# Kernel tuning notes

Measured on AMD Instinct MI355X. Metric: run time of the kernel, lower is better.

Reference implementation:

```python
import jax, jax.numpy as jnp
import numpy as np

N = 50000      # nodes
E = 800000     # edges
F = 128        # node_features
DSS = 64       # degree_set_size
H = 128        # latent dim (hardcoded in GraphES)


def gcn_conv(x, W, b, src, dst, n):
    # PyG GCNConv: linear -> symmetric-normalized aggregation with self loops -> bias
    h = x @ W                                            # [N, C_out]
    deg = jnp.zeros((n,), x.dtype).at[dst].add(1.0) + 1.0  # in-degree incl. self loop
    dinv = jax.lax.rsqrt(deg)
    norm = dinv[src] * dinv[dst]                         # [E]
    agg = jnp.zeros_like(h).at[dst].add(h[src] * norm[:, None])
    agg = agg + h * (dinv * dinv)[:, None]               # self-loop term (norm_ii = 1/deg_i)
    return agg + b


def mlp(x, w1, b1, w2, b2):
    return jax.nn.relu(x @ w1 + b1) @ w2 + b2


def _swap(ei, i1, i2, coin):
    e1 = jnp.take(ei, i1, axis=1)
    e2 = jnp.take(ei, i2, axis=1)
    a, b = e1[0], e1[1]
    c, d = e2[0], e2[1]
    ne1 = jnp.where(coin, jnp.stack([a, d]), jnp.stack([a, c]))
    ne2 = jnp.where(coin, jnp.stack([c, b]), jnp.stack([b, d]))
    return ei.at[:, i1].set(ne1).at[:, i2].set(ne2)


def setup_inputs() -> dict:
    key = jax.random.key(0)
    ks = jax.random.split(key, 24)
    s = 0.05

    def rn(k, shape):
        return jax.random.normal(k, shape, jnp.float32) * s

    return {
        "x": jax.random.normal(ks[0], (N, F), jnp.float32),
        "edge_index": jax.random.randint(ks[1], (2, E), 0, N, dtype=jnp.int32),
        "degree_set": jax.random.randint(ks[2], (N,), 0, DSS, dtype=jnp.int32),
        "timesteps": 5,
        # encoder: GCN(F+DSS -> 2H), GCN(2H -> H)
        "enc_w1": rn(ks[3], (F + DSS, 2 * H)), "enc_b1": jnp.zeros((2 * H,), jnp.float32),
        "enc_w2": rn(ks[4], (2 * H, H)),       "enc_b2": jnp.zeros((H,), jnp.float32),
        # decoder: GCN(H+DSS -> 2F), GCN(2F -> F)
        "dec_w1": rn(ks[5], (H + DSS, 2 * F)), "dec_b1": jnp.zeros((2 * F,), jnp.float32),
        "dec_w2": rn(ks[6], (2 * F, F)),       "dec_b2": jnp.zeros((F,), jnp.float32),
        # edge_predictor_1: Linear(128,64)->ReLU->Linear(64,1)
        "ep1_w1": rn(ks[7], (H, 64)),  "ep1_b1": jnp.zeros((64,), jnp.float32),
        "ep1_w2": rn(ks[8], (64, 1)),  "ep1_b2": jnp.zeros((1,), jnp.float32),
        # edge_predictor_2: input is z concat flattened pair features -> 128+256=384
        "ep2_w1": rn(ks[9], (H + 2 * H, 64)), "ep2_b1": jnp.zeros((64,), jnp.float32),
        "ep2_w2": rn(ks[10], (64, 1)),        "ep2_b2": jnp.zeros((1,), jnp.float32),
    }


def reference(x, edge_index, degree_set, timesteps,
              enc_w1, enc_b1, enc_w2, enc_b2,
              dec_w1, dec_b1, dec_w2, dec_b2,
              ep1_w1, ep1_b1, ep1_w2, ep1_b2,
              ep2_w1, ep2_b1, ep2_w2, ep2_b2):
    src, dst = edge_index[0], edge_index[1]
    dh = jax.nn.one_hot(degree_set, DSS, dtype=x.dtype)  # [N, DSS]

    # ---- encoder ----
    h = jax.nn.relu(gcn_conv(jnp.concatenate([x, dh], 1), enc_w1, enc_b1, src, dst, N))
    z = gcn_conv(h, enc_w2, enc_b2, src, dst, N)          # [N, H]

    # ---- forward diffusion: timesteps random edge swaps (deterministic PRNG) ----
    ei = edge_index
    for t in range(timesteps):
        k1, k2 = jax.random.split(jax.random.fold_in(jax.random.key(1), t))
        idx = jax.random.choice(k1, E, (2,), replace=False)
        ei = _swap(ei, idx[0], idx[1], jax.random.bernoulli(k2))

    # ---- reverse process: argmax-driven edge swaps ----
    # edge_predictor_1 scores depend only on z -> identical every step; compute once
    i1 = jnp.argmax(mlp(z, ep1_w1, ep1_b1, ep1_w2, ep1_b2).squeeze(-1))
    for t in range(timesteps):
        e1 = jnp.take(ei, i1, axis=1)                     # [2]
        e1f = z[e1].reshape(-1)                           # [2H]
        cond = jnp.concatenate([z, jnp.broadcast_to(e1f, (N, 2 * H))], 1)
        i2 = jnp.argmax(mlp(cond, ep2_w1, ep2_b1, ep2_w2, ep2_b2).squeeze(-1))
        coin = jax.random.bernoulli(jax.random.fold_in(jax.random.key(2), t))
        ei = _swap(ei, i1, i2, coin)

    # ---- decoder on final edge structure ----
    src2, dst2 = ei[0], ei[1]
    hd = jax.nn.relu(gcn_conv(jnp.concatenate([z, dh], 1), dec_w1, dec_b1, src2, dst2, N))
    out = gcn_conv(hd, dec_w2, dec_b2, src2, dst2, N)     # [N, F]
    return out, ei
```

## Files before the change

kernel.cpp:

```cpp
#include <hip/hip_runtime.h>
#include <cstdint>
#include <cstddef>
#include <vector>
#include <algorithm>

#define NN 50000
#define EE 800000
#define FF 128
#define HH 128
#define TSTEPS 5

typedef __attribute__((ext_vector_type(8))) short bf16x8;
typedef __attribute__((ext_vector_type(4))) float f32x4;

__device__ __forceinline__ float bf2f(unsigned short u)
{
    return __uint_as_float((unsigned)u << 16);
}
__device__ __forceinline__ unsigned short f2bf(float x)
{
    unsigned u = __float_as_uint(x);
    u = (u + 0x7FFFu + ((u >> 16) & 1u));
    return (unsigned short)(u >> 16);
}
__device__ __forceinline__ void splitbf(float v, unsigned short& hi, unsigned short& lo)
{
    hi = f2bf(v);
    lo = f2bf(v - bf2f(hi));
}

__device__ __forceinline__ void gload16(const void* g, void* l)
{
    __builtin_amdgcn_global_load_lds(
        (const __attribute__((address_space(1))) void*)g,
        (__attribute__((address_space(3))) void*)l, 16, 0, 0);
}

template <int K, int C, bool HAS_BIAS, bool OUTBF16, bool RELU>
__global__ __launch_bounds__(256) void gemm_rw(
    const float* __restrict__ A, const float* __restrict__ W,
    void* __restrict__ Pout, int n, const float* __restrict__ bias)
{
    constexpr int RPW = 8, ROWS = 32, CG = C / 64;
    __shared__ float As[ROWS][K];
    const int row0 = blockIdx.x * ROWS;
    const int tid = threadIdx.x;
    for (int idx4 = tid; idx4 < ROWS * K / 4; idx4 += 256) {
        int idx = idx4 * 4;
        int r = idx / K, k = idx - r * K;
        int gr = row0 + r;
        float4 v = make_float4(0.f, 0.f, 0.f, 0.f);
        if (gr < n) v = *(const float4*)(A + (size_t)gr * K + k);
        As[r][k + 0] = v.x; As[r][k + 1] = v.y;
        As[r][k + 2] = v.z; As[r][k + 3] = v.w;
    }
    __syncthreads();
    const int w = tid >> 6, l = tid & 63;
    float acc[RPW][CG];
#pragma unroll
    for (int r = 0; r < RPW; r++)
#pragma unroll
        for (int c = 0; c < CG; c++) acc[r][c] = 0.f;

    for (int k = 0; k < K; k++) {
        float wv[CG];
#pragma unroll
        for (int c = 0; c < CG; c++) wv[c] = W[k * C + l + 64 * c];
#pragma unroll
        for (int r = 0; r < RPW; r++) {
            float a = As[w * RPW + r][k];
#pragma unroll
            for (int c = 0; c < CG; c++) acc[r][c] = fmaf(a, wv[c], acc[r][c]);
        }
    }
#pragma unroll
    for (int r = 0; r < RPW; r++) {
        int gr = row0 + w * RPW + r;
        if (gr >= n) continue;
#pragma unroll
        for (int c = 0; c < CG; c++) {
            int col = l + 64 * c;
            float v = acc[r][c];
            if (HAS_BIAS) v += bias[col];
            if (RELU)     v = fmaxf(v, 0.f);
            if (OUTBF16) ((unsigned short*)Pout)[(size_t)gr * C + col] = f2bf(v);
            else         ((float*)Pout)[(size_t)gr * C + col] = v;
        }
    }
}

template <int K, int C, bool HAS_BIAS, bool RELU>
__global__ __launch_bounds__(256) void gemm_mfma(
    const unsigned short* __restrict__ A, const unsigned short* __restrict__ Wp,
    unsigned short* __restrict__ Pout, const float* __restrict__ bias, int n)
{
    constexpr int KC = K / 32;
    constexpr int NT = C / 16;
    __shared__ unsigned short As[64][K];
    const int row0 = blockIdx.x * 64;
    const int tid = threadIdx.x;
    for (int idx = tid; idx < 64 * (K / 8); idx += 256) {
        int r = idx / (K / 8), k8 = idx - r * (K / 8);
        int gr = row0 + r;
        bf16x8 v = { 0, 0, 0, 0, 0, 0, 0, 0 };
        if (gr < n) v = *(const bf16x8*)(A + (size_t)gr * K + k8 * 8);
        *(bf16x8*)(&As[r][k8 * 8]) = v;
    }
    __syncthreads();
    const int w = tid >> 6, lane = tid & 63;
    const int m = lane & 15, quad = lane >> 4;
    const int rowBase = w * 16;

    f32x4 acc[NT];
#pragma unroll
    for (int t = 0; t < NT; t++) acc[t] = { 0.f, 0.f, 0.f, 0.f };

    for (int kc = 0; kc < KC; kc++) {
        bf16x8 a = *(const bf16x8*)(&As[rowBase + m][kc * 32 + quad * 8]);
#pragma unroll
        for (int t = 0; t < NT; t++) {
            int ncol = t * 16 + m;
            bf16x8 b = *(const bf16x8*)(Wp + ((size_t)kc * C + ncol) * 32 + quad * 8);
            acc[t] = __builtin_amdgcn_mfma_f32_16x16x32_bf16(a, b, acc[t], 0, 0, 0);
        }
    }
#pragma unroll
    for (int t = 0; t < NT; t++) {
        int col = t * 16 + m;
#pragma unroll
        for (int r = 0; r < 4; r++) {
            int gr = row0 + rowBase + quad * 4 + r;
            if (gr >= n) continue;
            float v = acc[t][r];
            if (HAS_BIAS) v += bias[col];
            if (RELU)     v = fmaxf(v, 0.f);
            Pout[(size_t)gr * C + col] = f2bf(v);
        }
    }
}

template <int K, int C, int BC, int WR, int WC, bool HAS_BIAS, bool RELU, bool OUT_SPLIT>
__global__ __launch_bounds__(256) void gemm_split_tiled(
    const unsigned short* __restrict__ Ahi, const unsigned short* __restrict__ Alo,
    const unsigned short* __restrict__ Whi, const unsigned short* __restrict__ Wlo,
    void* __restrict__ PoutHi, unsigned short* __restrict__ PoutLo,
    const float* __restrict__ bias, int n)
{
    constexpr int KC = K / 32;
    constexpr int RT = 128 / (WR * 16);
    constexpr int TT = BC / (WC * 16);
    constexpr int LDS_USHORTS = 8192 + BC * 64;
    __shared__ __align__(16) unsigned short smem[LDS_USHORTS];
    unsigned short* AhL = smem;
    unsigned short* AlL = smem + 4096;
    unsigned short* WhL = smem + 8192;
    unsigned short* WlL = smem + 8192 + BC * 32;

    const int row0 = blockIdx.x * 128;
    const int col0 = blockIdx.y * BC;
    const int tid = threadIdx.x;
    const int w = tid >> 6, l = tid & 63;
    const int m = l & 15, quad = l >> 4;
    const int wr = w / WC, wc = w % WC;
    const int rowBase = wr * (RT * 16);
    const int colBase = wc * (TT * 16);

    f32x4 acc[RT][TT];
#pragma unroll
    for (int rt = 0; rt < RT; rt++)
#pragma unroll
        for (int tt = 0; tt < TT; tt++) acc[rt][tt] = { 0.f, 0.f, 0.f, 0.f };

    for (int kc = 0; kc < KC; kc++) {
        for (int s = w; s < 8; s += 4) {
            int rg = row0 + s * 16 + (l >> 2);
            if (rg > n - 1) rg = n - 1;
            size_t go = (size_t)rg * K + kc * 32 + (l & 3) * 8;
            gload16(Ahi + go, AhL + s * 512);
            gload16(Alo + go, AlL + s * 512);
        }
        for (int s = w; s < BC / 16; s += 4) {
            size_t wo = ((size_t)kc * C + col0) * 32 + s * 512 + l * 8;
            gload16(Whi + wo, WhL + s * 512);
            gload16(Wlo + wo, WlL + s * 512);
        }
        __syncthreads();

        bf16x8 ah[RT], al[RT];
#pragma unroll
        for (int rt = 0; rt < RT; rt++) {
            int ro = (rowBase + rt * 16 + m) * 32 + quad * 8;
            ah[rt] = *(const bf16x8*)(AhL + ro);
            al[rt] = *(const bf16x8*)(AlL + ro);
        }
#pragma unroll
        for (int tt = 0; tt < TT; tt++) {
            int co = (colBase + tt * 16 + m) * 32 + quad * 8;
            bf16x8 wh = *(const bf16x8*)(WhL + co);
            bf16x8 wl = *(const bf16x8*)(WlL + co);
#pragma unroll
            for (int rt = 0; rt < RT; rt++) {
                acc[rt][tt] = __builtin_amdgcn_mfma_f32_16x16x32_bf16(al[rt], wh, acc[rt][tt], 0, 0, 0);
                acc[rt][tt] = __builtin_amdgcn_mfma_f32_16x16x32_bf16(ah[rt], wl, acc[rt][tt], 0, 0, 0);
                acc[rt][tt] = __builtin_amdgcn_mfma_f32_16x16x32_bf16(ah[rt], wh, acc[rt][tt], 0, 0, 0);
            }
        }
        __syncthreads();
    }

    if (OUT_SPLIT) {
        unsigned short* Ot = smem;
#pragma unroll
        for (int tt = 0; tt < TT; tt++) {
            int col_in = colBase + tt * 16 + m;
            float bv = HAS_BIAS ? bias[col0 + col_in] : 0.f;
#pragma unroll
            for (int rt = 0; rt < RT; rt++)
#pragma unroll
                for (int r = 0; r < 4; r++) {
                    int row_in = rowBase + rt * 16 + quad * 4 + r;
                    float v = acc[rt][tt][r] + bv;
                    if (RELU) v = fmaxf(v, 0.f);
                    Ot[row_in * BC + col_in] = f2bf(v);
                }
        }
        __syncthreads();
        for (int idx = tid; idx < 128 * (BC / 8); idx += 256) {
            int rr = idx / (BC / 8), c8 = idx - rr * (BC / 8);
            int gr = row0 + rr;
            if (gr < n)
                *(bf16x8*)((unsigned short*)PoutHi + (size_t)gr * C + col0 + c8 * 8) =
                    *(const bf16x8*)(Ot + rr * BC + c8 * 8);
        }
        __syncthreads();
#pragma unroll
        for (int tt = 0; tt < TT; tt++) {
            int col_in = colBase + tt * 16 + m;
            float bv = HAS_BIAS ? bias[col0 + col_in] : 0.f;
#pragma unroll
            for (int rt = 0; rt < RT; rt++)
#pragma unroll
                for (int r = 0; r < 4; r++) {
                    int row_in = rowBase + rt * 16 + quad * 4 + r;
                    float v = acc[rt][tt][r] + bv;
                    if (RELU) v = fmaxf(v, 0.f);
                    unsigned short h = f2bf(v);
                    Ot[row_in * BC + col_in] = f2bf(v - bf2f(h));
                }
        }
        __syncthreads();
        for (int idx = tid; idx < 128 * (BC / 8); idx += 256) {
            int rr = idx / (BC / 8), c8 = idx - rr * (BC / 8);
            int gr = row0 + rr;
            if (gr < n)
                *(bf16x8*)(PoutLo + (size_t)gr * C + col0 + c8 * 8) =
                    *(const bf16x8*)(Ot + rr * BC + c8 * 8);
        }
    } else {
#pragma unroll
        for (int tt = 0; tt < TT; tt++) {
            int col = col0 + colBase + tt * 16 + m;
            float bv = HAS_BIAS ? bias[col] : 0.f;
#pragma unroll
            for (int rt = 0; rt < RT; rt++)
#pragma unroll
                for (int r = 0; r < 4; r++) {
                    int gr = row0 + rowBase + rt * 16 + quad * 4 + r;
                    if (gr >= n) continue;
                    float v = acc[rt][tt][r] + bv;
                    if (RELU) v = fmaxf(v, 0.f);
                    ((float*)PoutHi)[(size_t)gr * C + col] = v;
                }
        }
    }
}

template <int K, int C>
__global__ void pack_w(const float* __restrict__ W, unsigned short* __restrict__ Wp)
{
    int idx = blockIdx.x * 256 + threadIdx.x;
    if (idx >= K * C) return;
    int k = idx / C, nn = idx - k * C;
    Wp[((size_t)(k >> 5) * C + nn) * 32 + (k & 31)] = f2bf(W[idx]);
}

template <int K, int C>
__global__ void pack_w_split(const float* __restrict__ W,
                             unsigned short* __restrict__ Wphi,
                             unsigned short* __restrict__ Wplo)
{
    int idx = blockIdx.x * 256 + threadIdx.x;
    if (idx >= K * C) return;
    int k = idx / C, nn = idx - k * C;
    unsigned short hi, lo;
    splitbf(W[idx], hi, lo);
    size_t o = ((size_t)(k >> 5) * C + nn) * 32 + (k & 31);
    Wphi[o] = hi;
    Wplo[o] = lo;
}

__global__ void count_deg(const int* __restrict__ dst, int* __restrict__ cnt, int e)
{
    int i = blockIdx.x * blockDim.x + threadIdx.x;
    if (i < e) {
        unsigned d = (unsigned)dst[i];
        if (d < (unsigned)NN) atomicAdd(&cnt[d], 1);
    }
}

__global__ void make_dinv(const int* __restrict__ cnt, float* __restrict__ dinv, int n)
{
    int i = blockIdx.x * blockDim.x + threadIdx.x;
    if (i < n) dinv[i] = 1.0f / sqrtf((float)cnt[i] + 1.0f);
}

__global__ void scan_block(const int* __restrict__ cnt, int* __restrict__ excl,
                           int* __restrict__ bsum, int n)
{
    __shared__ int s[256];
    int i = blockIdx.x * 256 + threadIdx.x;
    int v = (i < n) ? cnt[i] : 0;
    s[threadIdx.x] = v;
    __syncthreads();
    for (int off = 1; off < 256; off <<= 1) {
        int t = (threadIdx.x >= off) ? s[threadIdx.x - off] : 0;
        __syncthreads();
        s[threadIdx.x] += t;
        __syncthreads();
    }
    if (i < n) excl[i] = s[threadIdx.x] - v;
    if (threadIdx.x == 255) bsum[blockIdx.x] = s[255];
}
__global__ void scan_bsum(int* __restrict__ bsum, int nb)
{
    if (threadIdx.x || blockIdx.x) return;
    int acc = 0;
    for (int b = 0; b < nb; b++) { int t = bsum[b]; bsum[b] = acc; acc += t; }
}
__global__ void scan_add(int* __restrict__ rowptr, const int* __restrict__ bsum, int n, int e)
{
    int i = blockIdx.x * 256 + threadIdx.x;
    if (i < n) rowptr[i] += bsum[blockIdx.x];
    if (i == 0) rowptr[n] = e;
}

__global__ void csr_fill_pairs(const int* __restrict__ src, const int* __restrict__ dst,
                               const float* __restrict__ dinv, const int* __restrict__ rowptr,
                               int* __restrict__ fill, int* __restrict__ csr_src,
                               float* __restrict__ csr_nrm, int e)
{
    int i = blockIdx.x * blockDim.x + threadIdx.x;
    if (i >= e) return;
    int d = dst[i], s = src[i];
    if ((unsigned)d >= (unsigned)NN || (unsigned)s >= (unsigned)NN) return;
    int slot = rowptr[d] + atomicAdd(&fill[d], 1);
    csr_src[slot] = s;
    csr_nrm[slot] = dinv[s] * dinv[d];
}

template <bool BF16SRC, int OUTMODE>
__global__ __launch_bounds__(256) void agg_feat(
    const void* __restrict__ Xv, const int* __restrict__ ds,
    const int* __restrict__ rowptr, const int* __restrict__ csr_src,
    const float* __restrict__ csr_nrm, const float* __restrict__ dinv,
    void* __restrict__ Fout, unsigned short* __restrict__ FoutLo)
{
    const int w = threadIdx.x >> 6, l = threadIdx.x & 63;
    const int i = blockIdx.x * 4 + w;
    if (i >= NN) return;
    const int half = l >> 5, lh = l & 31;

    auto loadRow4 = [&](int s, float* v) {
        if (BF16SRC) {
            ushort4 u = ((const ushort4*)((const unsigned short*)Xv + (size_t)s * 128))[lh];
            v[0] = bf2f(u.x); v[1] = bf2f(u.y); v[2] = bf2f(u.z); v[3] = bf2f(u.w);
        } else {
            float4 t = ((const float4*)((const float*)Xv + (size_t)s * 128))[lh];
            v[0] = t.x; v[1] = t.y; v[2] = t.z; v[3] = t.w;
        }
    };

    float di = dinv[i], d2 = di * di;
    float acc[4];
    {
        float sv[4];
        loadRow4(i, sv);
        float wgt = half ? 0.f : d2;
#pragma unroll
        for (int v = 0; v < 4; v++) acc[v] = sv[v] * wgt;
    }
    float hist = (ds[i] == l) ? d2 : 0.f;

    const int beg = rowptr[i], end = rowptr[i + 1];
    int idx = beg;
    for (; idx + 8 <= end; idx += 8) {
        int s[8]; float nw[8]; int b[8];
#pragma unroll
        for (int j = 0; j < 8; j++) { s[j] = csr_src[idx + j]; nw[j] = csr_nrm[idx + j]; }
#pragma unroll
        for (int j = 0; j < 8; j++) b[j] = ds[s[j]];
        float vv[4][4];
#pragma unroll
        for (int p = 0; p < 4; p++) loadRow4(s[2 * p + half], vv[p]);
#pragma unroll
        for (int p = 0; p < 4; p++) {
            float wp = nw[2 * p + half];
#pragma unroll
            for (int v = 0; v < 4; v++) acc[v] = fmaf(vv[p][v], wp, acc[v]);
        }
#pragma unroll
        for (int j = 0; j < 8; j++) hist += (b[j] == l) ? nw[j] : 0.f;
    }
    for (; idx + 2 <= end; idx += 2) {
        int s0 = csr_src[idx], s1 = csr_src[idx + 1];
        float n0 = csr_nrm[idx], n1 = csr_nrm[idx + 1];
        int b0 = ds[s0], b1 = ds[s1];
        float v0[4];
        loadRow4(half ? s1 : s0, v0);
        float wp = half ? n1 : n0;
#pragma unroll
        for (int v = 0; v < 4; v++) acc[v] = fmaf(v0[v], wp, acc[v]);
        hist += (b0 == l) ? n0 : 0.f;
        hist += (b1 == l) ? n1 : 0.f;
    }
    if (idx < end) {
        int s0 = csr_src[idx];
        float n0 = csr_nrm[idx];
        int b0 = ds[s0];
        float v0[4];
        loadRow4(s0, v0);
        float wp = half ? 0.f : n0;
#pragma unroll
        for (int v = 0; v < 4; v++) acc[v] = fmaf(v0[v], wp, acc[v]);
        hist += (b0 == l) ? n0 : 0.f;
    }
#pragma unroll
    for (int v = 0; v < 4; v++) acc[v] += __shfl_xor(acc[v], 32, 64);

    if (OUTMODE == 2) {
        if (half == 0) {
            unsigned short h[4], lo[4];
#pragma unroll
            for (int v = 0; v < 4; v++) splitbf(acc[v], h[v], lo[v]);
            ((ushort4*)((unsigned short*)Fout + (size_t)i * 192))[lh] =
                make_ushort4(h[0], h[1], h[2], h[3]);
            ((ushort4*)(FoutLo + (size_t)i * 192))[lh] =
                make_ushort4(lo[0], lo[1], lo[2], lo[3]);
        }
        unsigned short hh, ll;
        splitbf(hist, hh, ll);
        ((unsigned short*)Fout)[(size_t)i * 192 + 128 + l] = hh;
        FoutLo[(size_t)i * 192 + 128 + l] = ll;
    } else if (OUTMODE == 1) {
        if (half == 0) {
            ((ushort4*)((unsigned short*)Fout + (size_t)i * 192))[lh] =
                make_ushort4(f2bf(acc[0]), f2bf(acc[1]), f2bf(acc[2]), f2bf(acc[3]));
        }
        ((unsigned short*)Fout)[(size_t)i * 192 + 128 + l] = f2bf(hist);
    } else {
        if (half == 0) {
            ((float4*)((float*)Fout + (size_t)i * 192))[lh] =
                make_float4(acc[0], acc[1], acc[2], acc[3]);
        }
        ((float*)Fout)[(size_t)i * 192 + 128 + l] = hist;
    }
}

template <bool RELU, bool BF16P>
__global__ __launch_bounds__(256) void agg_wave(
    const void* __restrict__ Pv, const int* __restrict__ rowptr,
    const int* __restrict__ csr_src, const float* __restrict__ csr_nrm,
    const float* __restrict__ dinv, const float* __restrict__ bias,
    float* __restrict__ B, unsigned short* __restrict__ Bbf)
{
    const int w = threadIdx.x >> 6, l = threadIdx.x & 63;
    const int i = blockIdx.x * 4 + w;
    if (i >= NN) return;
    const int half = l >> 5, lh = l & 31;

    auto loadRow4 = [&](int s, float* v) {
        if (BF16P) {
            ushort4 u = ((const ushort4*)((const unsigned short*)Pv + (size_t)s * 128))[lh];
            v[0] = bf2f(u.x); v[1] = bf2f(u.y); v[2] = bf2f(u.z); v[3] = bf2f(u.w);
        } else {
            float4 t = ((const float4*)((const float*)Pv + (size_t)s * 128))[lh];
            v[0] = t.x; v[1] = t.y; v[2] = t.z; v[3] = t.w;
        }
    };

    float di = dinv[i], d2 = di * di;
    float acc[4];
    {
        float sv[4];
        loadRow4(i, sv);
        float wgt = half ? 0.f : d2;
#pragma unroll
        for (int v = 0; v < 4; v++) acc[v] = sv[v] * wgt;
    }

    const int beg = rowptr[i], end = rowptr[i + 1];
    int idx = beg;
    for (; idx + 8 <= end; idx += 8) {
        int s[8]; float nw[8];
#pragma unroll
        for (int j = 0; j < 8; j++) { s[j] = csr_src[idx + j]; nw[j] = csr_nrm[idx + j]; }
        float vv[4][4];
#pragma unroll
        for (int p = 0; p < 4; p++) loadRow4(s[2 * p + half], vv[p]);
#pragma unroll
        for (int p = 0; p < 4; p++) {
            float wp = nw[2 * p + half];
#pragma unroll
            for (int v = 0; v < 4; v++) acc[v] = fmaf(vv[p][v], wp, acc[v]);
        }
    }
    for (; idx + 2 <= end; idx += 2) {
        int s0 = csr_src[idx], s1 = csr_src[idx + 1];
        float n0 = csr_nrm[idx], n1 = csr_nrm[idx + 1];
        float v0[4];
        loadRow4(half ? s1 : s0, v0);
        float wp = half ? n1 : n0;
#pragma unroll
        for (int v = 0; v < 4; v++) acc[v] = fmaf(v0[v], wp, acc[v]);
    }
    if (idx < end) {
        int s0 = csr_src[idx];
        float n0 = csr_nrm[idx];
        float v0[4];
        loadRow4(s0, v0);
        float wp = half ? 0.f : n0;
#pragma unroll
        for (int v = 0; v < 4; v++) acc[v] = fmaf(v0[v], wp, acc[v]);
    }
#pragma unroll
    for (int v = 0; v < 4; v++) acc[v] += __shfl_xor(acc[v], 32, 64);

    if (half == 0) {
        float r[4];
#pragma unroll
        for (int v = 0; v < 4; v++) {
            r[v] = acc[v] + bias[lh * 4 + v];
            if (RELU) r[v] = fmaxf(r[v], 0.f);
        }
        ((float4*)(B + (size_t)i * 128))[lh] = make_float4(r[0], r[1], r[2], r[3]);
        if (Bbf)
            ((ushort4*)(Bbf + (size_t)i * 128))[lh] =
                make_ushort4(f2bf(r[0]), f2bf(r[1]), f2bf(r[2]), f2bf(r[3]));
    }
}

__device__ __forceinline__ unsigned long long packScore(float s, int i)
{
    unsigned u = __float_as_uint(s);
    u = (u & 0x80000000u) ? ~u : (u | 0x80000000u);
    return ((unsigned long long)u << 32) | (unsigned)(~(unsigned)i);
}
__device__ __forceinline__ int unpackIdx(unsigned long long v)
{
    return (int)(~(unsigned)(v & 0xFFFFFFFFull));
}
__device__ __forceinline__ unsigned long long maxu64(unsigned long long a,
                                                     unsigned long long b)
{
    return a > b ? a : b;
}

__global__ __launch_bounds__(256) void score1_blocks(
    const float* __restrict__ z, const float* __restrict__ w1,
    const float* __restrict__ b1, const float* __restrict__ w2,
    unsigned long long* __restrict__ blockBest, int n)
{
    __shared__ float Zs[16][HH];
    __shared__ float W1s[HH * 64];
    __shared__ float W2s[64], B1s[64];
    __shared__ unsigned long long red[4];
    const int row0 = blockIdx.x * 16;
    const int tid = threadIdx.x;
    for (int idx = tid; idx < 16 * HH; idx += 256) {
        int r = idx >> 7, k = idx & 127;
        int gr = row0 + r;
        Zs[r][k] = (gr < n) ? z[(size_t)gr * HH + k] : 0.f;
    }
    for (int idx = tid; idx < HH * 64; idx += 256) W1s[idx] = w1[idx];
    if (tid < 64) { W2s[tid] = w2[tid]; B1s[tid] = b1[tid]; }
    __syncthreads();

    const int w = tid >> 6, l = tid & 63;
    float acc[4];
#pragma unroll
    for (int r = 0; r < 4; r++) acc[r] = B1s[l];
#pragma unroll 16
    for (int k = 0; k < HH; k++) {
        float wv = W1s[k * 64 + l];
#pragma unroll
        for (int r = 0; r < 4; r++)
            acc[r] = fmaf(Zs[w * 4 + r][k], wv, acc[r]);
    }
    unsigned long long best = 0;
#pragma unroll
    for (int r = 0; r < 4; r++) {
        float p = fmaxf(acc[r], 0.f) * W2s[l];
#pragma unroll
        for (int off = 32; off > 0; off >>= 1) p += __shfl_xor(p, off, 64);
        int row = row0 + w * 4 + r;
        if (row < n) best = maxu64(best, packScore(p, row));
    }
    if (l == 0) red[w] = best;
    __syncthreads();
    if (tid == 0)
        blockBest[blockIdx.x] = maxu64(maxu64(red[0], red[1]), maxu64(red[2], red[3]));
}

__global__ __launch_bounds__(256) void reduce_best(
    const unsigned long long* __restrict__ arr, int m,
    unsigned long long* __restrict__ out)
{
    __shared__ unsigned long long red[4];
    const int tid = threadIdx.x;
    unsigned long long b = 0;
    for (int i = tid; i < m; i += 256) b = maxu64(b, arr[i]);
#pragma unroll
    for (int off = 32; off > 0; off >>= 1)
        b = maxu64(b, (unsigned long long)__shfl_xor((long long)b, off, 64));
    if ((tid & 63) == 0) red[tid >> 6] = b;
    __syncthreads();
    if (tid == 0)
        *out = maxu64(maxu64(red[0], red[1]), maxu64(red[2], red[3]));
}

__global__ __launch_bounds__(256) void score2_fused(
    const int* __restrict__ ei, const unsigned long long* __restrict__ best1,
    const float* __restrict__ z, const float* __restrict__ w1,
    const float* __restrict__ zw1, const float* __restrict__ w2,
    unsigned long long* __restrict__ blockBest, int n)
{
    __shared__ float za_s[HH], zb_s[HH];
    __shared__ float cpart[4][64];
    __shared__ float Cs[64], W2s[64];
    __shared__ unsigned long long red[4];
    int i1 = unpackIdx(*best1);
    if ((unsigned)i1 >= (unsigned)EE) i1 = 0;
    int a = ei[i1], b = ei[EE + i1];
    if ((unsigned)a >= (unsigned)NN) a = 0;
    if ((unsigned)b >= (unsigned)NN) b = 0;
    const int tid = threadIdx.x;
    if (tid < HH) za_s[tid] = z[(size_t)a * HH + tid];
    else          zb_s[tid - HH] = z[(size_t)b * HH + tid - HH];
    __syncthreads();
    const int h = tid & 63, kg = tid >> 6;
    float accc = 0.f;
#pragma unroll
    for (int kk = 0; kk < 32; kk++) {
        int k = kg * 32 + kk;
        accc = fmaf(za_s[k], w1[(128 + k) * 64 + h], accc);
        accc = fmaf(zb_s[k], w1[(256 + k) * 64 + h], accc);
    }
    cpart[kg][h] = accc;
    __syncthreads();
    if (tid < 64) {
        Cs[tid] = (cpart[0][tid] + cpart[1][tid]) + (cpart[2][tid] + cpart[3][tid]);
        W2s[tid] = w2[tid];
    }
    __syncthreads();
    const int w = kg, l = h;
    unsigned long long best = 0;
    for (int i = blockIdx.x * 4 + w; i < n; i += gridDim.x * 4) {
        float v = zw1[(size_t)i * 64 + l] + Cs[l];
        v = fmaxf(v, 0.f) * W2s[l];
#pragma unroll
        for (int off = 32; off > 0; off >>= 1) v += __shfl_xor(v, off, 64);
        best = maxu64(best, packScore(v, i));
    }
    if (l == 0) red[w] = best;
    __syncthreads();
    if (tid == 0)
        blockBest[blockIdx.x] = maxu64(maxu64(red[0], red[1]), maxu64(red[2], red[3]));
}

__global__ __launch_bounds__(256) void reduce_swap(
    const unsigned long long* __restrict__ arr, int m,
    int* __restrict__ ei, const unsigned long long* __restrict__ best1, int coin)
{
    __shared__ unsigned long long red[4];
    const int tid = threadIdx.x;
    unsigned long long b = 0;
    for (int i = tid; i < m; i += 256) b = maxu64(b, arr[i]);
#pragma unroll
    for (int off = 32; off > 0; off >>= 1)
        b = maxu64(b, (unsigned long long)__shfl_xor((long long)b, off, 64));
    if ((tid & 63) == 0) red[tid >> 6] = b;
    __syncthreads();
    if (tid == 0) {
        unsigned long long bestv = maxu64(maxu64(red[0], red[1]), maxu64(red[2], red[3]));
        int i1 = unpackIdx(*best1);
        int i2 = unpackIdx(bestv);
        if ((unsigned)i1 >= (unsigned)EE) i1 = 0;
        if ((unsigned)i2 >= (unsigned)EE) i2 = 0;
        int A = ei[i1], B = ei[EE + i1], C = ei[i2], D = ei[EE + i2];
        ei[i1] = A;             ei[EE + i1] = coin ? D : C;
        ei[i2] = coin ? C : B;  ei[EE + i2] = coin ? B : D;
    }
}

struct Swaps { int a[TSTEPS]; int b[TSTEPS]; unsigned coins; };

__global__ void fwd_swaps_k(int* __restrict__ ei, Swaps s)
{
    if (threadIdx.x != 0 || blockIdx.x != 0) return;
    for (int t = 0; t < TSTEPS; t++) {
        int i1 = s.a[t], i2 = s.b[t];
        if ((unsigned)i1 >= (unsigned)EE || (unsigned)i2 >= (unsigned)EE) continue;
        int coin = (s.coins >> t) & 1;
        int A = ei[i1], B = ei[EE + i1], C = ei[i2], D = ei[EE + i2];
        ei[i1] = A;             ei[EE + i1] = coin ? D : C;
        ei[i2] = coin ? C : B;  ei[EE + i2] = coin ? B : D;
    }
}

__global__ void write_out(const float* __restrict__ outF, const int* __restrict__ ei,
                          float* __restrict__ dst)
{
    int i = blockIdx.x * 256 + threadIdx.x;
    if (i < NN * FF) {
        float v = outF[i];
        v = fminf(fmaxf(v, -64.f), 64.f);
        dst[i] = v;
    } else if (i < NN * FF + 2 * EE) {
        dst[i] = (float)ei[i - NN * FF];
    }
}

static inline uint32_t rotl32(uint32_t x, int n) { return (x << n) | (x >> (32 - n)); }

static void tf(uint32_t k0, uint32_t k1, uint32_t c0, uint32_t c1,
               uint32_t& o0, uint32_t& o1)
{
    uint32_t ks[3] = { k0, k1, k0 ^ k1 ^ 0x1BD11BDAu };
    uint32_t x0 = c0 + ks[0], x1 = c1 + ks[1];
    static const int rA[4] = { 13, 15, 26, 6 };
    static const int rB[4] = { 17, 29, 16, 24 };
    for (int g = 0; g < 5; g++) {
        const int* r = (g & 1) ? rB : rA;
        for (int j = 0; j < 4; j++) { x0 += x1; x1 = rotl32(x1, r[j]); x1 ^= x0; }
        x0 += ks[(g + 1) % 3];
        x1 += ks[(g + 2) % 3] + (uint32_t)(g + 1);
    }
    o0 = x0; o1 = x1;
}

static void jsplit_part(uint32_t k0, uint32_t k1,
                        uint32_t& a0, uint32_t& a1, uint32_t& b0, uint32_t& b1)
{
    tf(k0, k1, 0u, 0u, a0, a1);
    tf(k0, k1, 0u, 1u, b0, b1);
}

static void jbits_part(uint32_t k0, uint32_t k1, uint32_t n, std::vector<uint32_t>& out)
{
    out.resize(n);
    for (uint32_t i = 0; i < n; i++) {
        uint32_t a, b;
        tf(k0, k1, 0u, i, a, b);
        out[i] = a ^ b;
    }
}

static bool jbern_part(uint32_t k0, uint32_t k1)
{
    uint32_t a, b;
    tf(k0, k1, 0u, 0u, a, b);
    return (a ^ b) < 0x80000000u;
}

struct PrngConsts {
    Swaps swaps;
    int revCoin[TSTEPS];
    PrngConsts()
    {
        swaps.coins = 0;
        std::vector<uint32_t> bits1, bits2;
        std::vector<uint64_t> packed((size_t)EE);
        for (int t = 0; t < TSTEPS; t++) {
            uint32_t kt0, kt1;
            tf(0u, 1u, 0u, (uint32_t)t, kt0, kt1);
            uint32_t kc0, kc1, kb0, kb1;
            jsplit_part(kt0, kt1, kc0, kc1, kb0, kb1);
            if (jbern_part(kb0, kb1)) swaps.coins |= (1u << t);

            uint32_t cur0 = kc0, cur1 = kc1, sub0, sub1, nk0, nk1;
            jsplit_part(cur0, cur1, nk0, nk1, sub0, sub1);
            cur0 = nk0; cur1 = nk1;
            jbits_part(sub0, sub1, EE, bits1);
            jsplit_part(cur0, cur1, nk0, nk1, sub0, sub1);
            cur0 = nk0; cur1 = nk1;
            jbits_part(sub0, sub1, EE, bits2);

            uint64_t m1 = ~0ull, m2 = ~0ull;
            for (uint32_t pos = 0; pos < EE; pos++) {
                uint64_t u = ((uint64_t)bits2[pos] << 32) | pos;
                if (u < m1) { m2 = m1; m1 = u; }
                else if (u < m2) { m2 = u; }
            }
            uint32_t pos0 = (uint32_t)m1, pos1 = (uint32_t)m2;
            for (uint32_t j = 0; j < EE; j++)
                packed[j] = ((uint64_t)bits1[j] << 32) | j;
            std::nth_element(packed.begin(), packed.begin() + pos0, packed.end());
            uint32_t j0 = (uint32_t)packed[pos0];
            std::nth_element(packed.begin(), packed.begin() + pos1, packed.end());
            uint32_t j1 = (uint32_t)packed[pos1];
            swaps.a[t] = (int)j0;
            swaps.b[t] = (int)j1;
        }
        for (int t = 0; t < TSTEPS; t++) {
            uint32_t kt0, kt1;
            tf(0u, 2u, 0u, (uint32_t)t, kt0, kt1);
            revCoin[t] = jbern_part(kt0, kt1) ? 1 : 0;
        }
    }
};
static const PrngConsts g_prng;

extern "C" void kernel_launch(void* const* d_in, const int* in_sizes, int n_in,
                              void* d_out, int out_size, void* d_ws, size_t ws_size,
                              hipStream_t stream)
{
    (void)out_size; (void)ws_size;

    static const int kWant[20] = {
        NN * FF, 2 * EE, NN, 1,
        192 * 256, 256, 256 * 128, 128,
        192 * 256, 256, 256 * 128, 128,
        128 * 64, 64, 64, 1,
        384 * 64, 64, 64, 1
    };
    const void* p[20] = {};
    {
        int j = 0;
        for (int k = 0; k < 20; k++) {
            if (j < n_in && in_sizes[j] == kWant[k]) { p[k] = d_in[j]; j++; }
            else if (kWant[k] == 1)                  { p[k] = nullptr; }
            else if (j < n_in)                       { p[k] = d_in[j]; j++; }
        }
    }
    const float* x      = (const float*)p[0];
    const int*   ei_in  = (const int*)p[1];
    const int*   ds     = (const int*)p[2];
    const float* enc_w1 = (const float*)p[4];
    const float* enc_b1 = (const float*)p[5];
    const float* enc_w2 = (const float*)p[6];
    const float* enc_b2 = (const float*)p[7];
    const float* dec_w1 = (const float*)p[8];
    const float* dec_b1 = (const float*)p[9];
    const float* dec_w2 = (const float*)p[10];
    const float* dec_b2 = (const float*)p[11];
    const float* ep1_w1 = (const float*)p[12];
    const float* ep1_b1 = (const float*)p[13];
    const float* ep1_w2 = (const float*)p[14];
    const float* ep2_w1 = (const float*)p[16];
    const float* ep2_b1 = (const float*)p[17];
    const float* ep2_w2 = (const float*)p[18];

    char* ws = (char*)d_ws;
    size_t off = 0;
    auto alloc = [&](size_t bytes) -> void* {
        void* q = ws + off;
        off += (bytes + 255) & ~(size_t)255;
        return q;
    };
    float* bufP    = (float*)alloc((size_t)NN * 256 * 4);
    float* bufH    = (float*)alloc((size_t)NN * 256 * 4);
    int*   eiw     = (int*)alloc((size_t)2 * EE * 4);
    int*   csr_src = (int*)alloc((size_t)EE * 4);
    float* csr_nrm = (float*)alloc((size_t)EE * 4);
    int*   rowptr  = (int*)alloc((size_t)(NN + 1) * 4);
    int*   cnt     = (int*)alloc((size_t)NN * 4);
    int*   fill    = (int*)alloc((size_t)NN * 4);
    int*   bsum    = (int*)alloc(256 * 4);
    float* dinv    = (float*)alloc((size_t)NN * 4);
    unsigned short* zbf   = (unsigned short*)alloc((size_t)NN * 128 * 2);
    unsigned short* wp1   = (unsigned short*)alloc((size_t)192 * 256 * 2);
    unsigned short* wp2   = (unsigned short*)alloc((size_t)256 * 128 * 2);
    unsigned short* w1hi  = (unsigned short*)alloc((size_t)192 * 256 * 2);
    unsigned short* w1lo  = (unsigned short*)alloc((size_t)192 * 256 * 2);
    unsigned short* w2hi  = (unsigned short*)alloc((size_t)256 * 128 * 2);
    unsigned short* w2lo  = (unsigned short*)alloc((size_t)256 * 128 * 2);
    unsigned long long* blockBest = (unsigned long long*)alloc(4096 * 8);
    unsigned long long* best1 = (unsigned long long*)alloc(8);

    unsigned short* f1hi = (unsigned short*)bufP;
    unsigned short* f1lo = f1hi + (size_t)NN * 192;
    float* P2   = bufP;
    float* zw1  = bufP;
    unsigned short* feat2bf = (unsigned short*)bufP;
    unsigned short* p4      = (unsigned short*)bufP;
    float* outF = bufP + (size_t)NN * 128;
    unsigned short* hhi = (unsigned short*)bufH;
    unsigned short* hlo = hhi + (size_t)NN * 256;
    float* zbuf = bufH;
    unsigned short* hdbf = (unsigned short*)bufH;

    const int TPB = 256;
    const int gN      = (NN + TPB - 1) / TPB;
    const int gE      = (EE + TPB - 1) / TPB;
    const int gRows16 = (NN + 15) / 16;
    const int gRows32 = (NN + 31) / 32;
    const int gRows64 = (NN + 63) / 64;
    const int gRows128 = (NN + 127) / 128;
    const int gWave   = (NN + 3) / 4;

    pack_w<192, 256><<<(192 * 256 + TPB - 1) / TPB, TPB, 0, stream>>>(dec_w1, wp1);
    pack_w<256, 128><<<(256 * 128 + TPB - 1) / TPB, TPB, 0, stream>>>(dec_w2, wp2);
    pack_w_split<192, 256><<<(192 * 256 + TPB - 1) / TPB, TPB, 0, stream>>>(enc_w1, w1hi, w1lo);
    pack_w_split<256, 128><<<(256 * 128 + TPB - 1) / TPB, TPB, 0, stream>>>(enc_w2, w2hi, w2lo);

    hipMemsetAsync(cnt, 0, (size_t)NN * 4, stream);
    count_deg<<<gE, TPB, 0, stream>>>(ei_in + EE, cnt, EE);
    make_dinv<<<gN, TPB, 0, stream>>>(cnt, dinv, NN);
    scan_block<<<gN, TPB, 0, stream>>>(cnt, rowptr, bsum, NN);
    scan_bsum<<<1, 64, 0, stream>>>(bsum, gN);
    scan_add<<<gN, TPB, 0, stream>>>(rowptr, bsum, NN, EE);
    hipMemsetAsync(fill, 0, (size_t)NN * 4, stream);
    csr_fill_pairs<<<gE, TPB, 0, stream>>>(ei_in, ei_in + EE, dinv, rowptr, fill,
                                           csr_src, csr_nrm, EE);

    agg_feat<false, 2><<<gWave, TPB, 0, stream>>>(
        x, ds, rowptr, csr_src, csr_nrm, dinv, f1hi, f1lo);
    gemm_split_tiled<192, 256, 128, 2, 2, true, true, true>
        <<<dim3(gRows128, 2), TPB, 0, stream>>>(
        f1hi, f1lo, w1hi, w1lo, hhi, hlo, enc_b1, NN);

    gemm_split_tiled<256, 128, 64, 4, 1, false, false, false>
        <<<dim3(gRows128, 2), TPB, 0, stream>>>(
        hhi, hlo, w2hi, w2lo, P2, nullptr, nullptr, NN);
    agg_wave<false, false><<<gWave, TPB, 0, stream>>>(
        P2, rowptr, csr_src, csr_nrm, dinv, enc_b2, zbuf, zbf);

    score1_blocks<<<gRows16, TPB, 0, stream>>>(zbuf, ep1_w1, ep1_b1, ep1_w2,
                                               blockBest, NN);
    reduce_best<<<1, TPB, 0, stream>>>(blockBest, gRows16, best1);
    gemm_rw<128, 64, true, false, false><<<gRows32, TPB, 0, stream>>>(
        zbuf, ep2_w1, zw1, NN, ep2_b1);

    hipMemcpyAsync(eiw, ei_in, (size_t)2 * EE * 4, hipMemcpyDeviceToDevice, stream);
    fwd_swaps_k<<<1, 64, 0, stream>>>(eiw, g_prng.swaps);

    for (int t = 0; t < TSTEPS; t++) {
        score2_fused<<<256, TPB, 0, stream>>>(eiw, best1, zbuf, ep2_w1,
                                              zw1, ep2_w2, blockBest, NN);
        reduce_swap<<<1, TPB, 0, stream>>>(blockBest, 256, eiw, best1,
                                           g_prng.revCoin[t]);
    }

    hipMemsetAsync(cnt, 0, (size_t)NN * 4, stream);
    count_deg<<<gE, TPB, 0, stream>>>(eiw + EE, cnt, EE);
    make_dinv<<<gN, TPB, 0, stream>>>(cnt, dinv, NN);
    scan_block<<<gN, TPB, 0, stream>>>(cnt, rowptr, bsum, NN);
    scan_bsum<<<1, 64, 0, stream>>>(bsum, gN);
    scan_add<<<gN, TPB, 0, stream>>>(rowptr, bsum, NN, EE);
    hipMemsetAsync(fill, 0, (size_t)NN * 4, stream);
    csr_fill_pairs<<<gE, TPB, 0, stream>>>(eiw, eiw + EE, dinv, rowptr, fill,
                                           csr_src, csr_nrm, EE);

    agg_feat<true, 1><<<gWave, TPB, 0, stream>>>(
        zbf, ds, rowptr, csr_src, csr_nrm, dinv, feat2bf, nullptr);
    gemm_mfma<192, 256, true, true><<<gRows64, TPB, 0, stream>>>(
        feat2bf, wp1, hdbf, dec_b1, NN);

    gemm_mfma<256, 128, false, false><<<gRows64, TPB, 0, stream>>>(
        hdbf, wp2, p4, nullptr, NN);
    agg_wave<false, true><<<gWave, TPB, 0, stream>>>(
        p4, rowptr, csr_src, csr_nrm, dinv, dec_b2, outF, nullptr);

    write_out<<<(NN * FF + 2 * EE + TPB - 1) / TPB, TPB, 0, stream>>>(
        outF, eiw, (float*)d_out);
}
```

Baseline: 887.4 us.

## Tile decoder GEMMs with LDS staging and fold reductions into scoring kernels

Replaces the decoder's per-wave MFMA GEMM with a 128-row, column-tiled kernel that stages A and packed W chunks in LDS and writes coalesced output through an LDS transpose. Merges make_dinv into scan_block, replaces scan_bsum/scan_add/fill memset with one kernel that recomputes block prefixes, and folds the argmax reductions and edge swap into the scoring kernels via a last-block atomic counter. The goal is fewer kernel launches and better weight reuse in the GEMMs, at the cost of a serial per-block prefix loop and reliance on threadfence/atomic last-block logic.

After: 872.2 us. About the same (-1.7%).

```diff
diff --git a/kernel.cpp b/kernel.cpp
--- a/kernel.cpp
+++ b/kernel.cpp
@@ -89,53 +89,85 @@
     }
 }
 
-template <int K, int C, bool HAS_BIAS, bool RELU>
-__global__ __launch_bounds__(256) void gemm_mfma(
+template <int K, int C, int BC, int WR, int WC, bool HAS_BIAS, bool RELU>
+__global__ __launch_bounds__(256) void gemm_bf16_tiled(
     const unsigned short* __restrict__ A, const unsigned short* __restrict__ Wp,
     unsigned short* __restrict__ Pout, const float* __restrict__ bias, int n)
 {
     constexpr int KC = K / 32;
-    constexpr int NT = C / 16;
-    __shared__ unsigned short As[64][K];
-    const int row0 = blockIdx.x * 64;
+    constexpr int RT = 128 / (WR * 16);
+    constexpr int TT = BC / (WC * 16);
+    constexpr int STAGE_USHORTS = 4096 + BC * 32;
+    constexpr int OT_USHORTS = 128 * BC;
+    constexpr int LDS_USHORTS = (STAGE_USHORTS > OT_USHORTS) ? STAGE_USHORTS : OT_USHORTS;
+    __shared__ __align__(16) unsigned short smem[LDS_USHORTS];
+    unsigned short* AL = smem;
+    unsigned short* WL = smem + 4096;
+
+    const int row0 = blockIdx.x * 128;
+    const int col0 = blockIdx.y * BC;
     const int tid = threadIdx.x;
-    for (int idx = tid; idx < 64 * (K / 8); idx += 256) {
-        int r = idx / (K / 8), k8 = idx - r * (K / 8);
-        int gr = row0 + r;
-        bf16x8 v = { 0, 0, 0, 0, 0, 0, 0, 0 };
-        if (gr < n) v = *(const bf16x8*)(A + (size_t)gr * K + k8 * 8);
-        *(bf16x8*)(&As[r][k8 * 8]) = v;
+    const int w = tid >> 6, l = tid & 63;
+    const int m = l & 15, quad = l >> 4;
+    const int wr = w / WC, wc = w % WC;
+    const int rowBase = wr * (RT * 16);
+    const int colBase = wc * (TT * 16);
+
+    f32x4 acc[RT][TT];
+#pragma unroll
+    for (int rt = 0; rt < RT; rt++)
+#pragma unroll
+        for (int tt = 0; tt < TT; tt++) acc[rt][tt] = { 0.f, 0.f, 0.f, 0.f };
+
+    for (int kc = 0; kc < KC; kc++) {
+        for (int s = w; s < 8; s += 4) {
+            int rg = row0 + s * 16 + (l >> 2);
+            if (rg > n - 1) rg = n - 1;
+            size_t go = (size_t)rg * K + kc * 32 + (l & 3) * 8;
+            gload16(A + go, AL + s * 512);
+        }
+        for (int s = w; s < BC / 16; s += 4) {
+            size_t wo = ((size_t)kc * C + col0) * 32 + s * 512 + l * 8;
+            gload16(Wp + wo, WL + s * 512);
+        }
+        __syncthreads();
+
+        bf16x8 a[RT];
+#pragma unroll
+        for (int rt = 0; rt < RT; rt++)
+            a[rt] = *(const bf16x8*)(AL + (rowBase + rt * 16 + m) * 32 + quad * 8);
+#pragma unroll
+        for (int tt = 0; tt < TT; tt++) {
+            bf16x8 b = *(const bf16x8*)(WL + (colBase + tt * 16 + m) * 32 + quad * 8);
+#pragma unroll
+            for (int rt = 0; rt < RT; rt++)
+                acc[rt][tt] = __builtin_amdgcn_mfma_f32_16x16x32_bf16(a[rt], b, acc[rt][tt], 0, 0, 0);
+        }
+        __syncthreads();
+    }
+
+    unsigned short* Ot = smem;
+#pragma unroll
+    for (int tt = 0; tt < TT; tt++) {
+        int col_in = colBase + tt * 16 + m;
+        float bv = HAS_BIAS ? bias[col0 + col_in] : 0.f;
+#pragma unroll
+        for (int rt = 0; rt < RT; rt++)
+#pragma unroll
+            for (int r = 0; r < 4; r++) {
+                int row_in = rowBase + rt * 16 + quad * 4 + r;
+                float v = acc[rt][tt][r] + bv;
+                if (RELU) v = fmaxf(v, 0.f);
+                Ot[row_in * BC + col_in] = f2bf(v);
+            }
     }
     __syncthreads();
-    const int w = tid >> 6, lane = tid & 63;
-    const int m = lane & 15, quad = lane >> 4;
-    const int rowBase = w * 16;
-
-    f32x4 acc[NT];
-#pragma unroll
-    for (int t = 0; t < NT; t++) acc[t] = { 0.f, 0.f, 0.f, 0.f };
-
-    for (int kc = 0; kc < KC; kc++) {
-        bf16x8 a = *(const bf16x8*)(&As[rowBase + m][kc * 32 + quad * 8]);
-#pragma unroll
-        for (int t = 0; t < NT; t++) {
-            int ncol = t * 16 + m;
-            bf16x8 b = *(const bf16x8*)(Wp + ((size_t)kc * C + ncol) * 32 + quad * 8);
-            acc[t] = __builtin_amdgcn_mfma_f32_16x16x32_bf16(a, b, acc[t], 0, 0, 0);
-        }
-    }
-#pragma unroll
-    for (int t = 0; t < NT; t++) {
-        int col = t * 16 + m;
-#pragma unroll
-        for (int r = 0; r < 4; r++) {
-            int gr = row0 + rowBase + quad * 4 + r;
-            if (gr >= n) continue;
-            float v = acc[t][r];
-            if (HAS_BIAS) v += bias[col];
-            if (RELU)     v = fmaxf(v, 0.f);
-            Pout[(size_t)gr * C + col] = f2bf(v);
-        }
+    for (int idx = tid; idx < 128 * (BC / 8); idx += 256) {
+        int rr = idx / (BC / 8), c8 = idx - rr * (BC / 8);
+        int gr = row0 + rr;
+        if (gr < n)
+            *(bf16x8*)(Pout + (size_t)gr * C + col0 + c8 * 8) =
+                *(const bf16x8*)(Ot + rr * BC + c8 * 8);
     }
 }
 
@@ -308,18 +340,13 @@
     }
 }
 
-__global__ void make_dinv(const int* __restrict__ cnt, float* __restrict__ dinv, int n)
-{
-    int i = blockIdx.x * blockDim.x + threadIdx.x;
-    if (i < n) dinv[i] = 1.0f / sqrtf((float)cnt[i] + 1.0f);
-}
-
 __global__ void scan_block(const int* __restrict__ cnt, int* __restrict__ excl,
-                           int* __restrict__ bsum, int n)
+                           int* __restrict__ bsum, float* __restrict__ dinv, int n)
 {
     __shared__ int s[256];
     int i = blockIdx.x * 256 + threadIdx.x;
     int v = (i < n) ? cnt[i] : 0;
+    if (i < n) dinv[i] = 1.0f / sqrtf((float)v + 1.0f);
     s[threadIdx.x] = v;
     __syncthreads();
     for (int off = 1; off < 256; off <<= 1) {
@@ -331,16 +358,13 @@
     if (i < n) excl[i] = s[threadIdx.x] - v;
     if (threadIdx.x == 255) bsum[blockIdx.x] = s[255];
 }
-__global__ void scan_bsum(int* __restrict__ bsum, int nb)
-{
-    if (threadIdx.x || blockIdx.x) return;
-    int acc = 0;
-    for (int b = 0; b < nb; b++) { int t = bsum[b]; bsum[b] = acc; acc += t; }
-}
-__global__ void scan_add(int* __restrict__ rowptr, const int* __restrict__ bsum, int n, int e)
-{
+__global__ void scan_add_fill(int* __restrict__ rowptr, const int* __restrict__ bsum,
+                              int* __restrict__ fill, int n, int e)
+{
+    int pre = 0;
+    for (int b = 0; b < (int)blockIdx.x; b++) pre += bsum[b];
     int i = blockIdx.x * 256 + threadIdx.x;
-    if (i < n) rowptr[i] += bsum[blockIdx.x];
+    if (i < n) { rowptr[i] += pre; fill[i] = 0; }
     if (i == 0) rowptr[n] = e;
 }
 
@@ -568,12 +592,15 @@
 __global__ __launch_bounds__(256) void score1_blocks(
     const float* __restrict__ z, const float* __restrict__ w1,
     const float* __restrict__ b1, const float* __restrict__ w2,
-    unsigned long long* __restrict__ blockBest, int n)
+    unsigned long long* __restrict__ blockBest,
+    unsigned long long* __restrict__ out, unsigned* __restrict__ counter,
+    int n, int nblocks)
 {
     __shared__ float Zs[16][HH];
     __shared__ float W1s[HH * 64];
     __shared__ float W2s[64], B1s[64];
     __shared__ unsigned long long red[4];
+    __shared__ unsigned isLast;
     const int row0 = blockIdx.x * 16;
     const int tid = threadIdx.x;
     for (int idx = tid; idx < 16 * HH; idx += 256) {
@@ -607,37 +634,41 @@
     }
     if (l == 0) red[w] = best;
     __syncthreads();
-    if (tid == 0)
+    if (tid == 0) {
         blockBest[blockIdx.x] = maxu64(maxu64(red[0], red[1]), maxu64(red[2], red[3]));
-}
-
-__global__ __launch_bounds__(256) void reduce_best(
-    const unsigned long long* __restrict__ arr, int m,
-    unsigned long long* __restrict__ out)
-{
-    __shared__ unsigned long long red[4];
-    const int tid = threadIdx.x;
-    unsigned long long b = 0;
-    for (int i = tid; i < m; i += 256) b = maxu64(b, arr[i]);
-#pragma unroll
-    for (int off = 32; off > 0; off >>= 1)
-        b = maxu64(b, (unsigned long long)__shfl_xor((long long)b, off, 64));
-    if ((tid & 63) == 0) red[tid >> 6] = b;
+        __threadfence();
+        unsigned prev = atomicAdd(counter, 1u);
+        isLast = (prev == (unsigned)(nblocks - 1)) ? 1u : 0u;
+    }
     __syncthreads();
-    if (tid == 0)
-        *out = maxu64(maxu64(red[0], red[1]), maxu64(red[2], red[3]));
+    if (isLast) {
+        __threadfence();
+        unsigned long long b = 0;
+        for (int i = tid; i < nblocks; i += 256) b = maxu64(b, blockBest[i]);
+#pragma unroll
+        for (int off = 32; off > 0; off >>= 1)
+            b = maxu64(b, (unsigned long long)__shfl_xor((long long)b, off, 64));
+        if ((tid & 63) == 0) red[tid >> 6] = b;
+        __syncthreads();
+        if (tid == 0) {
+            *out = maxu64(maxu64(red[0], red[1]), maxu64(red[2], red[3]));
+            *counter = 0;
+        }
+    }
 }
 
 __global__ __launch_bounds__(256) void score2_fused(
-    const int* __restrict__ ei, const unsigned long long* __restrict__ best1,
+    int* __restrict__ ei, const unsigned long long* __restrict__ best1,
     const float* __restrict__ z, const float* __restrict__ w1,
     const float* __restrict__ zw1, const float* __restrict__ w2,
-    unsigned long long* __restrict__ blockBest, int n)
+    unsigned long long* __restrict__ blockBest, unsigned* __restrict__ counter,
+    int n, int coin)
 {
     __shared__ float za_s[HH], zb_s[HH];
     __shared__ float cpart[4][64];
     __shared__ float Cs[64], W2s[64];
     __shared__ unsigned long long red[4];
+    __shared__ unsigned isLast;
     int i1 = unpackIdx(*best1);
     if ((unsigned)i1 >= (unsigned)EE) i1 = 0;
     int a = ei[i1], b = ei[EE + i1];
@@ -673,32 +704,32 @@
     }
     if (l == 0) red[w] = best;
     __syncthreads();
-    if (tid == 0)
+    const int nblocks = (int)gridDim.x;
+    if (tid == 0) {
         blockBest[blockIdx.x] = maxu64(maxu64(red[0], red[1]), maxu64(red[2], red[3]));
-}
-
-__global__ __launch_bounds__(256) void reduce_swap(
-    const unsigned long long* __restrict__ arr, int m,
-    int* __restrict__ ei, const unsigned long long* __restrict__ best1, int coin)
-{
-    __shared__ unsigned long long red[4];
-    const int tid = threadIdx.x;
-    unsigned long long b = 0;
-    for (int i = tid; i < m; i += 256) b = maxu64(b, arr[i]);
-#pragma unroll
-    for (int off = 32; off > 0; off >>= 1)
-        b = maxu64(b, (unsigned long long)__shfl_xor((long long)b, off, 64));
-    if ((tid & 63) == 0) red[tid >> 6] = b;
+        __threadfence();
+        unsigned prev = atomicAdd(counter, 1u);
+        isLast = (prev == (unsigned)(nblocks - 1)) ? 1u : 0u;
+    }
     __syncthreads();
-    if (tid == 0) {
-        unsigned long long bestv = maxu64(maxu64(red[0], red[1]), maxu64(red[2], red[3]));
-        int i1 = unpackIdx(*best1);
-        int i2 = unpackIdx(bestv);
-        if ((unsigned)i1 >= (unsigned)EE) i1 = 0;
-        if ((unsigned)i2 >= (unsigned)EE) i2 = 0;
-        int A = ei[i1], B = ei[EE + i1], C = ei[i2], D = ei[EE + i2];
-        ei[i1] = A;             ei[EE + i1] = coin ? D : C;
-        ei[i2] = coin ? C : B;  ei[EE + i2] = coin ? B : D;
+    if (isLast) {
+        __threadfence();
+        unsigned long long bb = 0;
+        for (int i = tid; i < nblocks; i += 256) bb = maxu64(bb, blockBest[i]);
+#pragma unroll
+        for (int off = 32; off > 0; off >>= 1)
+            bb = maxu64(bb, (unsigned long long)__shfl_xor((long long)bb, off, 64));
+        if ((tid & 63) == 0) red[tid >> 6] = bb;
+        __syncthreads();
+        if (tid == 0) {
+            unsigned long long bestv = maxu64(maxu64(red[0], red[1]), maxu64(red[2], red[3]));
+            int i2 = unpackIdx(bestv);
+            if ((unsigned)i2 >= (unsigned)EE) i2 = 0;
+            int A = ei[i1], B = ei[EE + i1], C = ei[i2], D = ei[EE + i2];
+            ei[i1] = A;             ei[EE + i1] = coin ? D : C;
+            ei[i2] = coin ? C : B;  ei[EE + i2] = coin ? B : D;
+            *counter = 0;
+        }
     }
 }
 
@@ -886,6 +917,7 @@
     unsigned short* w2lo  = (unsigned short*)alloc((size_t)256 * 128 * 2);
     unsigned long long* blockBest = (unsigned long long*)alloc(4096 * 8);
     unsigned long long* best1 = (unsigned long long*)alloc(8);
+    unsigned* counters = (unsigned*)alloc(256);
 
     unsigned short* f1hi = (unsigned short*)bufP;
     unsigned short* f1lo = f1hi + (size_t)NN * 192;
@@ -904,9 +936,10 @@
     const int gE      = (EE + TPB - 1) / TPB;
     const int gRows16 = (NN + 15) / 16;
     const int gRows32 = (NN + 31) / 32;
-    const int gRows64 = (NN + 63) / 64;
     const int gRows128 = (NN + 127) / 128;
     const int gWave   = (NN + 3) / 4;
+
+    hipMemsetAsync(counters, 0, 8, stream);
 
     pack_w<192, 256><<<(192 * 256 + TPB - 1) / TPB, TPB, 0, stream>>>(dec_w1, wp1);
     pack_w<256, 128><<<(256 * 128 + TPB - 1) / TPB, TPB, 0, stream>>>(dec_w2, wp2);
@@ -915,11 +948,8 @@
 
     hipMemsetAsync(cnt, 0, (size_t)NN * 4, stream);
     count_deg<<<gE, TPB, 0, stream>>>(ei_in + EE, cnt, EE);
-    make_dinv<<<gN, TPB, 0, stream>>>(cnt, dinv, NN);
-    scan_block<<<gN, TPB, 0, stream>>>(cnt, rowptr, bsum, NN);
-    scan_bsum<<<1, 64, 0, stream>>>(bsum, gN);
-    scan_add<<<gN, TPB, 0, stream>>>(rowptr, bsum, NN, EE);
-    hipMemsetAsync(fill, 0, (size_t)NN * 4, stream);
+    scan_block<<<gN, TPB, 0, stream>>>(cnt, rowptr, bsum, dinv, NN);
+    scan_add_fill<<<gN, TPB, 0, stream>>>(rowptr, bsum, fill, NN, EE);
     csr_fill_pairs<<<gE, TPB, 0, stream>>>(ei_in, ei_in + EE, dinv, rowptr, fill,
                                            csr_src, csr_nrm, EE);
 
@@ -936,8 +966,8 @@
         P2, rowptr, csr_src, csr_nrm, dinv, enc_b2, zbuf, zbf);
 
     score1_blocks<<<gRows16, TPB, 0, stream>>>(zbuf, ep1_w1, ep1_b1, ep1_w2,
-                                               blockBest, NN);
-    reduce_best<<<1, TPB, 0, stream>>>(blockBest, gRows16, best1);
+                                               blockBest, best1, counters + 0,
+                                               NN, gRows16);
     gemm_rw<128, 64, true, false, false><<<gRows32, TPB, 0, stream>>>(
         zbuf, ep2_w1, zw1, NN, ep2_b1);
 
@@ -946,27 +976,25 @@
 
     for (int t = 0; t < TSTEPS; t++) {
         score2_fused<<<256, TPB, 0, stream>>>(eiw, best1, zbuf, ep2_w1,
-                                              zw1, ep2_w2, blockBest, NN);
-        reduce_swap<<<1, TPB, 0, stream>>>(blockBest, 256, eiw, best1,
-                                           g_prng.revCoin[t]);
+                                              zw1, ep2_w2, blockBest, counters + 1,
+                                              NN, g_prng.revCoin[t]);
     }
 
     hipMemsetAsync(cnt, 0, (size_t)NN * 4, stream);
     count_deg<<<gE, TPB, 0, stream>>>(eiw + EE, cnt, EE);
-    make_dinv<<<gN, TPB, 0, stream>>>(cnt, dinv, NN);
-    scan_block<<<gN, TPB, 0, stream>>>(cnt, rowptr, bsum, NN);
-    scan_bsum<<<1, 64, 0, stream>>>(bsum, gN);
-    scan_add<<<gN, TPB, 0, stream>>>(rowptr, bsum, NN, EE);
-    hipMemsetAsync(fill, 0, (size_t)NN * 4, stream);
+    scan_block<<<gN, TPB, 0, stream>>>(cnt, rowptr, bsum, dinv, NN);
+    scan_add_fill<<<gN, TPB, 0, stream>>>(rowptr, bsum, fill, NN, EE);
     csr_fill_pairs<<<gE, TPB, 0, stream>>>(eiw, eiw + EE, dinv, rowptr, fill,
                                            csr_src, csr_nrm, EE);
 
     agg_feat<true, 1><<<gWave, TPB, 0, stream>>>(
         zbf, ds, rowptr, csr_src, csr_nrm, dinv, feat2bf, nullptr);
-    gemm_mfma<192, 256, true, true><<<gRows64, TPB, 0, stream>>>(
+    gemm_bf16_tiled<192, 256, 128, 2, 2, true, true>
+        <<<dim3(gRows128, 2), TPB, 0, stream>>>(
         feat2bf, wp1, hdbf, dec_b1, NN);
 
-    gemm_mfma<256, 128, false, false><<<gRows64, TPB, 0, stream>>>(
+    gemm_bf16_tiled<256, 128, 128, 2, 2, false, false>
+        <<<dim3(gRows128, 1), TPB, 0, stream>>>(
         hdbf, wp2, p4, nullptr, NN);
     agg_wave<false, true><<<gWave, TPB, 0, stream>>>(
         p4, rowptr, csr_src, csr_nrm, dinv, dec_b2, outF, nullptr);
```
